# Optimization experiments

Measured on AMD Instinct MI355X. Metric: run time of the kernel, lower is better.

Reference implementation:

```python
import jax, jax.numpy as jnp
import numpy as np
from jax import lax

N, CIN, H, W = 4, 1024, 56, 56
CB = 256          # bottleneck channels
K = 9             # 3x3 kernel taps


def _conv(x, w, b, stride=1, padding='SAME'):
    y = lax.conv_general_dilated(x, w, (stride, stride), padding,
                                 dimension_numbers=('NCHW', 'OIHW', 'NCHW'))
    return y + b[None, :, None, None]


def _bilinear_gather(feat, ys, xs):
    # feat: [N,C,H,W]; ys, xs: [N,P] float sample coords. Zero padding outside.
    n, c, h, w = feat.shape
    y0 = jnp.floor(ys); x0 = jnp.floor(xs)
    wy1 = ys - y0; wy0 = 1.0 - wy1
    wx1 = xs - x0; wx0 = 1.0 - wx1
    flat = feat.reshape(n, c, h * w)

    def g(yi, xi):
        valid = (yi >= 0) & (yi <= h - 1) & (xi >= 0) & (xi <= w - 1)
        yc = jnp.clip(yi, 0, h - 1).astype(jnp.int32)
        xc = jnp.clip(xi, 0, w - 1).astype(jnp.int32)
        idx = (yc * w + xc)  # [N,P]
        vals = jnp.take_along_axis(flat, idx[:, None, :], axis=2)  # [N,C,P]
        return vals * valid[:, None, :].astype(feat.dtype)

    out = (g(y0, x0) * (wy0 * wx0)[:, None, :]
           + g(y0, x0 + 1) * (wy0 * wx1)[:, None, :]
           + g(y0 + 1, x0) * (wy1 * wx0)[:, None, :]
           + g(y0 + 1, x0 + 1) * (wy1 * wx1)[:, None, :])
    return out  # [N,C,P]


def _deform_conv3x3(feat, w, b, w_off, b_off):
    # DCNv1: offsets predicted by a standard 3x3 conv (18 = 2*K channels),
    # then bilinear-sample input at p + p_k + offset, accumulate with kernel w.
    n, c, h, ww = feat.shape
    off = _conv(feat, w_off, b_off)                 # [N, 2K, H, W]
    off = off.reshape(n, K, 2, h, ww)
    dy, dx = off[:, :, 0], off[:, :, 1]             # [N,K,H,W]
    ki, kj = jnp.meshgrid(jnp.arange(3), jnp.arange(3), indexing='ij')
    ky = (ki.reshape(-1) - 1).astype(feat.dtype)    # kernel dy offsets, rate=1
    kx = (kj.reshape(-1) - 1).astype(feat.dtype)
    hh = jnp.arange(h, dtype=feat.dtype)
    wc = jnp.arange(ww, dtype=feat.dtype)
    ys = hh[None, None, :, None] + ky[None, :, None, None] + dy   # [N,K,H,W]
    xs = wc[None, None, None, :] + kx[None, :, None, None] + dx
    sampled = _bilinear_gather(feat, ys.reshape(n, -1), xs.reshape(n, -1))
    sampled = sampled.reshape(n, c, K, h, ww)       # [N,C,K,H,W]
    out = jnp.einsum('nckhw,ock->nohw', sampled, w.reshape(w.shape[0], c, K))
    return out + b[None, :, None, None]


def setup_inputs() -> dict:
    key = jax.random.key(0)
    ks = jax.random.split(key, 6)
    x = jax.random.normal(ks[0], (N, CIN, H, W), dtype=jnp.float32)
    w1 = jax.random.normal(ks[1], (CB, CIN, 1, 1), dtype=jnp.float32) * 0.02
    b1 = jnp.zeros((CB,), jnp.float32)
    w_off = jax.random.normal(ks[2], (2 * K, CB, 3, 3), dtype=jnp.float32) * 0.01
    b_off = jnp.zeros((2 * K,), jnp.float32)
    w2 = jax.random.normal(ks[3], (CB, CB, 3, 3), dtype=jnp.float32) * 0.02
    b2 = jnp.zeros((CB,), jnp.float32)
    w3 = jax.random.normal(ks[4], (CIN, CB, 1, 1), dtype=jnp.float32) * 0.02
    b3 = jnp.zeros((CIN,), jnp.float32)
    return {"x": x, "w1": w1, "b1": b1, "w_off": w_off, "b_off": b_off,
            "w2": w2, "b2": b2, "w3": w3, "b3": b3}


def reference(x, w1, b1, w_off, b_off, w2, b2, w3, b3):
    # shortcut is identity (in_channels == out_channels, stride=1)
    r = jax.nn.relu(_conv(x, w1, b1))                      # conv1 1x1 + relu
    r = jax.nn.relu(_deform_conv3x3(r, w2, b2, w_off, b_off))  # deform 3x3 + relu
    r = _conv(r, w3, b3)                                   # conv3 1x1, no act
    return jax.nn.relu(x + r)
```

## Files before the change

kernel.cpp:

```cpp
#include <hip/hip_runtime.h>
#include <hip/hip_bf16.h>

#define N_   4
#define CIN  1024
#define H_   56
#define W_   56
#define HW   3136
#define CB   256
#define KK   9
#define OFFC 18

typedef __attribute__((ext_vector_type(8))) short short8;
typedef __attribute__((ext_vector_type(4))) short short4v;
typedef __attribute__((ext_vector_type(4))) float float4v;
typedef unsigned short ushort_t;

__device__ inline ushort_t bf16_rne(float f) {
    unsigned int u = __float_as_uint(f);
    unsigned int r = (u + 0x7FFFu + ((u >> 16) & 1u)) >> 16;
    return (ushort_t)r;
}
__device__ inline void split_bf16(float f, ushort_t& hi, ushort_t& lo) {
    ushort_t h = bf16_rne(f);
    float hf = __uint_as_float(((unsigned int)h) << 16);
    hi = h;
    lo = bf16_rne(f - hf);
}
__device__ inline short8 ld_frag_lds(const ushort_t* base) {
    short4v a = *(const short4v*)base;
    short4v b = *(const short4v*)(base + 4);
    return __builtin_shufflevector(a, b, 0, 1, 2, 3, 4, 5, 6, 7);
}
__device__ inline void lds_barrier() {
    asm volatile("s_waitcnt lgkmcnt(0)" ::: "memory");
    __builtin_amdgcn_s_barrier();
    __builtin_amdgcn_sched_barrier(0);
}

__global__ void __launch_bounds__(256) pack_weights_kernel(
    const float* __restrict__ w1, const float* __restrict__ w2,
    const float* __restrict__ w3, const float* __restrict__ w_off,
    ushort_t* __restrict__ w1p, ushort_t* __restrict__ w2p,
    ushort_t* __restrict__ w3p, ushort_t* __restrict__ wofp)
{
    int e = blockIdx.x * 256 + threadIdx.x;
    if (e < 256 * 1024) {
        int o = e >> 10, k = e & 1023;
        ushort_t hi, lo; split_bf16(w1[e], hi, lo);
        w1p[(size_t)(o * 2 + 0) * 1024 + k] = hi;
        w1p[(size_t)(o * 2 + 1) * 1024 + k] = lo;
        return;
    }
    e -= 256 * 1024;
    if (e < 256 * 256 * 9) {
        int o = e / 2304; int rem = e % 2304; int c = rem / 9; int k = rem % 9;
        w2p[(size_t)(k * 256 + o) * 256 + c] = bf16_rne(w2[e]);
        return;
    }
    e -= 256 * 256 * 9;
    if (e < 1024 * 256) {
        int o = e >> 8, k = e & 255;
        ushort_t hi, lo; split_bf16(w3[e], hi, lo);
        w3p[(size_t)(o * 2 + 0) * 256 + k] = hi;
        w3p[(size_t)(o * 2 + 1) * 256 + k] = lo;
        return;
    }
    e -= 1024 * 256;
    if (e < 9 * 32 * 256) {
        int k = e / (32 * 256);
        int rem = e % (32 * 256);
        int m = rem >> 8, c = rem & 255;
        float v = (m < OFFC) ? w_off[((size_t)m * 256 + c) * 9 + k] : 0.f;
        wofp[e] = bf16_rne(v);
    }
}

template <int MFRAG, bool RELU, bool RESID>
__global__ void __launch_bounds__(256, 4) conv1x1_mfma_kernel(
    const ushort_t* __restrict__ Wp,
    const float* __restrict__ Xin,
    const float* __restrict__ bias,
    const float* __restrict__ resid,
    float* __restrict__ Cout,
    int M, int Kdim)
{
    __shared__ ushort_t Bs[64][36];

    const int tid  = threadIdx.x;
    const int wave = tid >> 6;
    const int lane = tid & 63;
    const int l15  = lane & 15;
    const int quad = lane >> 4;
    const int pBase = blockIdx.x * 64;
    const int mBase = blockIdx.y * (MFRAG * 64) + wave * (MFRAG * 16);
    const int n     = blockIdx.z;
    const float* Xn = Xin + (size_t)n * Kdim * HW;

    float4v acc[MFRAG][4];
#pragma unroll
    for (int i = 0; i < MFRAG; ++i)
#pragma unroll
        for (int j = 0; j < 4; ++j) acc[i][j] = (float4v)(0.f);

    const int kk = tid >> 3;
    const int pq = (tid & 7) * 8;

    const float* src0 = &Xn[(size_t)kk * HW + pBase + pq];
    float4 c0 = *reinterpret_cast<const float4*>(src0);
    float4 c1 = *reinterpret_cast<const float4*>(src0 + 4);

    for (int k0 = 0; k0 < Kdim; k0 += 32) {
        lds_barrier();
        float vs[8] = {c0.x, c0.y, c0.z, c0.w, c1.x, c1.y, c1.z, c1.w};
#pragma unroll
        for (int j = 0; j < 8; ++j) Bs[pq + j][kk] = bf16_rne(vs[j]);

        short8 ah[MFRAG], al[MFRAG];
#pragma unroll
        for (int mt = 0; mt < MFRAG; ++mt) {
            const ushort_t* arow = Wp +
                ((size_t)(mBase + mt * 16 + l15) * 2) * Kdim + k0 + quad * 8;
            ah[mt] = *(const short8*)(arow);
            al[mt] = *(const short8*)(arow + Kdim);
        }
        if (k0 + 32 < Kdim) {
            const float* src = &Xn[(size_t)(k0 + 32 + kk) * HW + pBase + pq];
            c0 = *reinterpret_cast<const float4*>(src);
            c1 = *reinterpret_cast<const float4*>(src + 4);
        }
        lds_barrier();

        short8 bh[4];
#pragma unroll
        for (int nt = 0; nt < 4; ++nt)
            bh[nt] = ld_frag_lds(&Bs[nt * 16 + l15][quad * 8]);
        __builtin_amdgcn_s_setprio(1);
#pragma unroll
        for (int mt = 0; mt < MFRAG; ++mt)
#pragma unroll
            for (int nt = 0; nt < 4; ++nt) {
                acc[mt][nt] = __builtin_amdgcn_mfma_f32_16x16x32_bf16(
                    ah[mt], bh[nt], acc[mt][nt], 0, 0, 0);
                acc[mt][nt] = __builtin_amdgcn_mfma_f32_16x16x32_bf16(
                    al[mt], bh[nt], acc[mt][nt], 0, 0, 0);
            }
        __builtin_amdgcn_s_setprio(0);
    }

#pragma unroll
    for (int mt = 0; mt < MFRAG; ++mt)
#pragma unroll
        for (int rr = 0; rr < 4; ++rr) {
            int row = mBase + mt * 16 + quad * 4 + rr;
            float bv = bias[row];
#pragma unroll
            for (int nt = 0; nt < 4; ++nt) {
                int col = pBase + nt * 16 + l15;
                size_t idx = ((size_t)n * M + row) * HW + col;
                float v = acc[mt][nt][rr] + bv;
                if (RESID) v += resid[idx];
                if (RELU)  v = fmaxf(v, 0.f);
                Cout[idx] = v;
            }
        }
}

__global__ void __launch_bounds__(256, 2) offset_mfma_kernel(
    const float* __restrict__ r,
    const ushort_t* __restrict__ wofp,
    const float* __restrict__ b_off,
    float* __restrict__ off)
{
    __shared__ float win[32][174];

    const int tid  = threadIdx.x;
    const int h    = blockIdx.x;
    const int n    = blockIdx.y;
    const int wave = tid >> 6;
    const int lane = tid & 63;
    const int l15  = lane & 15;
    const int quad = lane >> 4;
    const float* rn = r + (size_t)n * CB * HW;

    const int p = wave * 16 + l15;

    float4v acc[2];
    acc[0] = (float4v)(0.f);
    acc[1] = (float4v)(0.f);

    for (int cb = 0; cb < CB; cb += 32) {
        __syncthreads();
        for (int f = tid; f < 32 * 3 * 14; f += 256) {
            int c = f / 42, remf = f % 42, row = remf / 14, x4 = (remf % 14) * 4;
            int yg = h - 1 + row;
            float4 v = {0.f, 0.f, 0.f, 0.f};
            if (yg >= 0 && yg < H_)
                v = *reinterpret_cast<const float4*>(
                    &rn[(size_t)(cb + c) * HW + yg * W_ + x4]);
            *reinterpret_cast<float4*>(&win[c][row * 56 + x4]) = v;
        }
        __syncthreads();

        short8 ahA0, ahA1, ahB0, ahB1;
        {
            const ushort_t* a0 = wofp + (size_t)(0 * 32 + l15) * 256 + cb + quad * 8;
            ahA0 = *(const short8*)a0;
            ahA1 = *(const short8*)(a0 + 16 * 256);
        }
#pragma unroll
        for (int k = 0; k < KK; ++k) {
            if (k + 1 < KK) {
                const ushort_t* a1 = wofp +
                    (size_t)((k + 1) * 32 + l15) * 256 + cb + quad * 8;
                ahB0 = *(const short8*)a1;
                ahB1 = *(const short8*)(a1 + 16 * 256);
            }
            const int ky = k / 3;
            const int dx = (k % 3) - 1;
            int x = p + dx;
            bool pvalid = (p < 56) && (x >= 0) && (x < 56);
            int xc = min(max(x, 0), 55);
            short8 bh;
#pragma unroll
            for (int j = 0; j < 8; ++j) {
                float v = win[quad * 8 + j][ky * 56 + xc];
                bh[j] = (short)bf16_rne(pvalid ? v : 0.f);
            }
            acc[0] = __builtin_amdgcn_mfma_f32_16x16x32_bf16(
                ahA0, bh, acc[0], 0, 0, 0);
            acc[1] = __builtin_amdgcn_mfma_f32_16x16x32_bf16(
                ahA1, bh, acc[1], 0, 0, 0);
            ahA0 = ahB0; ahA1 = ahB1;
        }
    }

    if (p < 56) {
#pragma unroll
        for (int mt = 0; mt < 2; ++mt)
#pragma unroll
            for (int rr = 0; rr < 4; ++rr) {
                int m = mt * 16 + quad * 4 + rr;
                if (m < OFFC)
                    off[((size_t)n * OFFC + m) * HW + h * W_ + p] =
                        acc[mt][rr] + b_off[m];
            }
    }
}

#define TPX   28
#define WROWS 5
#define WCOLS 36
#define WPOS  (WROWS * WCOLS)
#define CSTR  33
#define WITEMS (32 * WROWS * 9)
#define DBLK  (H_ * 2 * N_)
#define NCHUNK 8

__global__ void __launch_bounds__(512, 2) deform_mfma_kernel(
    const float* __restrict__ r,
    const float* __restrict__ off,
    const ushort_t* __restrict__ w2p,
    const float* __restrict__ b2,
    float* __restrict__ r2)
{
    __shared__ float    win[WPOS][CSTR];
    __shared__ ushort_t Bs[2][KK][32][36];

    const int tid = threadIdx.x;
    const int bid = blockIdx.x;
    const int swz = (bid & 7) * (DBLK >> 3) + (bid >> 3);
    const int xh  = swz & 1;
    const int h   = (swz >> 1) % H_;
    const int n   = swz / (H_ * 2);
    const int xb  = xh * TPX;
    const float* rn   = r + (size_t)n * CB * HW;
    const float* offn = off + (size_t)n * OFFC * HW;

    int   bi0 = 0, bi1 = 0, bi2 = 0, bi3 = 0;
    float bw0 = 0.f, bw1 = 0.f, bw2 = 0.f, bw3 = 0.f;
    int   go0 = 0, go1 = 0, go2 = 0, go3 = 0;
    bool  bfast = true;
    const bool bactive = (tid < 288);
    const int  bk = bactive ? (tid / 32) : 0;
    const int  bp = bactive ? (tid % 32) : 0;
    if (bactive && bp < TPX) {
        int pg = xb + bp;
        float dy = offn[(size_t)(2 * bk) * HW + h * W_ + pg];
        float dx = offn[(size_t)(2 * bk + 1) * HW + h * W_ + pg];
        float ys = (float)(h + (bk / 3) - 1) + dy;
        float xs = (float)(pg + (bk % 3) - 1) + dx;
        float y0f = floorf(ys), x0f = floorf(xs);
        int y0 = (int)y0f, x0 = (int)x0f;
        float wy1 = ys - y0f, wy0 = 1.f - wy1;
        float wx1 = xs - x0f, wx0 = 1.f - wx1;
        int   wid[4]; float wg[4]; int gof[4]; bool fast = true;
#pragma unroll
        for (int u = 0; u < 2; ++u)
#pragma unroll
            for (int vv = 0; vv < 2; ++vv) {
                int yy = y0 + u, xx = x0 + vv;
                bool valid = (yy >= 0) && (yy <= 55) && (xx >= 0) && (xx <= 55);
                float wgt = valid ? (u ? wy1 : wy0) * (vv ? wx1 : wx0) : 0.f;
                int ry = yy - (h - 2);
                int rx = xx - (xb - 4);
                if (wgt != 0.f &&
                    (ry < 0 || ry >= WROWS || rx < 0 || rx >= WCOLS))
                    fast = false;
                int idx = min(max(ry, 0), WROWS - 1) * WCOLS +
                          min(max(rx, 0), WCOLS - 1);
                wid[u * 2 + vv] = idx;
                wg[u * 2 + vv]  = wgt;
                gof[u * 2 + vv] = valid ? (yy * W_ + xx) : 0;
            }
        bfast = fast;
        bi0 = wid[0]; bi1 = wid[1]; bi2 = wid[2]; bi3 = wid[3];
        bw0 = wg[0];  bw1 = wg[1];  bw2 = wg[2];  bw3 = wg[3];
        go0 = gof[0]; go1 = gof[1]; go2 = gof[2]; go3 = gof[3];
    }

    const int wave = tid >> 6;
    const int lane = tid & 63;
    const int l15  = lane & 15;
    const int quad = lane >> 4;
    const int mW   = wave * 32;

    float4v acc[2][2];
#pragma unroll
    for (int i = 0; i < 2; ++i)
#pragma unroll
        for (int j = 0; j < 2; ++j) acc[i][j] = (float4v)(0.f);

    auto wload = [&](int f, int cbg) -> float4 {
        int c = f / 45, remf = f % 45, row = remf / 9, q = remf % 9;
        int yg = min(max(h - 2 + row, 0), H_ - 1);
        int xg = xb - 4 + q * 4;
        const float* src = &rn[(size_t)(cbg + c) * HW + yg * W_];
        float4 v;
        if (xg >= 0 && xg <= W_ - 4) {
            v = *reinterpret_cast<const float4*>(src + xg);
        } else {
            v.x = src[min(max(xg + 0, 0), W_ - 1)];
            v.y = src[min(max(xg + 1, 0), W_ - 1)];
            v.z = src[min(max(xg + 2, 0), W_ - 1)];
            v.w = src[min(max(xg + 3, 0), W_ - 1)];
        }
        return v;
    };
    auto wwrite = [&](float4* pre) {
#pragma unroll
        for (int i = 0; i < 3; ++i) {
            int f = tid + 512 * i;
            if (f < WITEMS) {
                int c = f / 45, remf = f % 45, row = remf / 9, q = remf % 9;
                int pos = row * WCOLS + q * 4;
                float4 v = pre[i];
                win[pos + 0][c] = v.x;
                win[pos + 1][c] = v.y;
                win[pos + 2][c] = v.z;
                win[pos + 3][c] = v.w;
            }
        }
    };
    auto build = [&](int cbg, int pb) {
#pragma unroll
        for (int c4 = 0; c4 < 32; c4 += 4) {
            float s[4];
            if (bfast) {
#pragma unroll
                for (int j = 0; j < 4; ++j) {
                    int c = c4 + j;
                    s[j] = bw0 * win[bi0][c] + bw1 * win[bi1][c] +
                           bw2 * win[bi2][c] + bw3 * win[bi3][c];
                }
            } else {
#pragma unroll
                for (int j = 0; j < 4; ++j) {
                    const float* rc = rn + (size_t)(cbg + c4 + j) * HW;
                    s[j] = bw0 * rc[go0] + bw1 * rc[go1] +
                           bw2 * rc[go2] + bw3 * rc[go3];
                }
            }
            short4v pk;
#pragma unroll
            for (int j = 0; j < 4; ++j) pk[j] = (short)bf16_rne(s[j]);
            *(short4v*)&Bs[pb][bk][bp][c4] = pk;
        }
    };

    float4 pre[3];
#pragma unroll
    for (int i = 0; i < 3; ++i) {
        int f = tid + 512 * i;
        if (f < WITEMS) pre[i] = wload(f, 0);
    }
    wwrite(pre);
#pragma unroll
    for (int i = 0; i < 3; ++i) {
        int f = tid + 512 * i;
        if (f < WITEMS) pre[i] = wload(f, 32);
    }
    lds_barrier();
    if (bactive) build(0, 0);
    lds_barrier();

    for (int ci = 0; ci < NCHUNK; ++ci) {
        const int cb = ci * 32;
        const bool hasNext = (ci + 1 < NCHUNK);
        if (hasNext) {
            wwrite(pre);
            if (ci + 2 < NCHUNK) {
#pragma unroll
                for (int i = 0; i < 3; ++i) {
                    int f = tid + 512 * i;
                    if (f < WITEMS) pre[i] = wload(f, cb + 64);
                }
            }
            lds_barrier();
            if (bactive) build(cb + 32, (ci + 1) & 1);
        }

        const ushort_t* bsb = &Bs[ci & 1][0][0][0];
        __builtin_amdgcn_s_setprio(1);
#pragma unroll
        for (int k = 0; k < KK; ++k) {
            short8 ah[2];
#pragma unroll
            for (int mt = 0; mt < 2; ++mt) {
                const ushort_t* arow = w2p +
                    (size_t)(k * 256 + (mW + mt * 16 + l15)) * 256 +
                    cb + quad * 8;
                ah[mt] = *(const short8*)(arow);
            }
            short8 bh[2];
#pragma unroll
            for (int nt = 0; nt < 2; ++nt)
                bh[nt] = ld_frag_lds(bsb + ((size_t)k * 32 +
                         nt * 16 + l15) * 36 + quad * 8);
#pragma unroll
            for (int mt = 0; mt < 2; ++mt)
#pragma unroll
                for (int nt = 0; nt < 2; ++nt)
                    acc[mt][nt] = __builtin_amdgcn_mfma_f32_16x16x32_bf16(
                        ah[mt], bh[nt], acc[mt][nt], 0, 0, 0);
        }
        __builtin_amdgcn_s_setprio(0);
        if (hasNext) lds_barrier();
    }

#pragma unroll
    for (int mt = 0; mt < 2; ++mt)
#pragma unroll
        for (int rr = 0; rr < 4; ++rr) {
            int o = mW + mt * 16 + quad * 4 + rr;
            float bv = b2[o];
#pragma unroll
            for (int nt = 0; nt < 2; ++nt) {
                int p = nt * 16 + l15;
                if (p < TPX) {
                    float v = fmaxf(acc[mt][nt][rr] + bv, 0.f);
                    r2[((size_t)n * CB + o) * HW + h * W_ + xb + p] = v;
                }
            }
        }
}

extern "C" void kernel_launch(void* const* d_in, const int* in_sizes, int n_in,
                              void* d_out, int out_size, void* d_ws, size_t ws_size,
                              hipStream_t stream)
{
    const float* x     = (const float*)d_in[0];
    const float* w1    = (const float*)d_in[1];
    const float* b1    = (const float*)d_in[2];
    const float* w_off = (const float*)d_in[3];
    const float* b_off = (const float*)d_in[4];
    const float* w2    = (const float*)d_in[5];
    const float* b2    = (const float*)d_in[6];
    const float* w3    = (const float*)d_in[7];
    const float* b3    = (const float*)d_in[8];
    float* out = (float*)d_out;

    float* ws  = (float*)d_ws;
    float* r    = ws;
    float* r2   = r  + (size_t)N_ * CB * HW;
    float* offb = r2 + (size_t)N_ * CB * HW;
    ushort_t* w1p  = (ushort_t*)(offb + (size_t)N_ * OFFC * HW);
    ushort_t* w2p  = w1p + (size_t)256 * 2 * 1024;
    ushort_t* w3p  = w2p + (size_t)9 * 256 * 256;
    ushort_t* wofp = w3p + (size_t)1024 * 2 * 256;

    {
        int total = 256 * 1024 + 256 * 256 * 9 + 1024 * 256 + 9 * 32 * 256;
        pack_weights_kernel<<<(total + 255) / 256, 256, 0, stream>>>(
            w1, w2, w3, w_off, w1p, w2p, w3p, wofp);
    }
    {
        dim3 grid(HW / 64, CB / 128, N_);
        conv1x1_mfma_kernel<2, true, false><<<grid, 256, 0, stream>>>(
            w1p, x, b1, nullptr, r, CB, CIN);
    }
    {
        dim3 grid(H_, N_);
        offset_mfma_kernel<<<grid, 256, 0, stream>>>(r, wofp, b_off, offb);
    }
    {
        deform_mfma_kernel<<<DBLK, 512, 0, stream>>>(r, offb, w2p, b2, r2);
    }
    {
        dim3 grid(HW / 64, CIN / 128, N_);
        conv1x1_mfma_kernel<2, true, true><<<grid, 256, 0, stream>>>(
            w3p, r2, b3, x, out, CIN, CB);
    }
}
```

Before: 341.6 us.

## Split offset conv over input-channel halves and shrink conv1 M tile

The offset conv grid is split along input channels into two halves, doubling its block count from 224 to 448. Each half writes its own partial sum buffer, and the deform kernel adds the two partials plus the bias when it reads the offsets. Separately, conv1 now uses a 64-row M tile instead of 128, which also doubles its block count and should fill the GPU better. The cost is an extra partial-offset buffer with the extra reads that come with it, and more redundant loading of B tiles in conv1.

```diff
diff --git a/kernel.cpp b/kernel.cpp
--- a/kernel.cpp
+++ b/kernel.cpp
@@ -168,19 +168,20 @@
 __global__ void __launch_bounds__(256, 2) offset_mfma_kernel(
     const float* __restrict__ r,
     const ushort_t* __restrict__ wofp,
-    const float* __restrict__ b_off,
-    float* __restrict__ off)
+    float* __restrict__ offp)
 {
     __shared__ float win[32][174];
 
     const int tid  = threadIdx.x;
     const int h    = blockIdx.x;
-    const int n    = blockIdx.y;
+    const int kh   = blockIdx.y;
+    const int n    = blockIdx.z;
     const int wave = tid >> 6;
     const int lane = tid & 63;
     const int l15  = lane & 15;
     const int quad = lane >> 4;
     const float* rn = r + (size_t)n * CB * HW;
+    const int cb0 = kh * 128;
 
     const int p = wave * 16 + l15;
 
@@ -188,7 +189,7 @@
     acc[0] = (float4v)(0.f);
     acc[1] = (float4v)(0.f);
 
-    for (int cb = 0; cb < CB; cb += 32) {
+    for (int cb = cb0; cb < cb0 + 128; cb += 32) {
         __syncthreads();
         for (int f = tid; f < 32 * 3 * 14; f += 256) {
             int c = f / 42, remf = f % 42, row = remf / 14, x4 = (remf % 14) * 4;
@@ -235,14 +236,14 @@
     }
 
     if (p < 56) {
+        float* base = offp + (size_t)(kh * N_ + n) * OFFC * HW;
 #pragma unroll
         for (int mt = 0; mt < 2; ++mt)
 #pragma unroll
             for (int rr = 0; rr < 4; ++rr) {
                 int m = mt * 16 + quad * 4 + rr;
                 if (m < OFFC)
-                    off[((size_t)n * OFFC + m) * HW + h * W_ + p] =
-                        acc[mt][rr] + b_off[m];
+                    base[(size_t)m * HW + h * W_ + p] = acc[mt][rr];
             }
     }
 }
@@ -259,6 +260,7 @@
 __global__ void __launch_bounds__(512, 2) deform_mfma_kernel(
     const float* __restrict__ r,
     const float* __restrict__ off,
+    const float* __restrict__ b_off,
     const ushort_t* __restrict__ w2p,
     const float* __restrict__ b2,
     float* __restrict__ r2)
@@ -273,8 +275,9 @@
     const int h   = (swz >> 1) % H_;
     const int n   = swz / (H_ * 2);
     const int xb  = xh * TPX;
-    const float* rn   = r + (size_t)n * CB * HW;
-    const float* offn = off + (size_t)n * OFFC * HW;
+    const float* rn    = r + (size_t)n * CB * HW;
+    const float* offn0 = off + (size_t)n * OFFC * HW;
+    const float* offn1 = off + (size_t)(N_ + n) * OFFC * HW;
 
     int   bi0 = 0, bi1 = 0, bi2 = 0, bi3 = 0;
     float bw0 = 0.f, bw1 = 0.f, bw2 = 0.f, bw3 = 0.f;
@@ -285,8 +288,10 @@
     const int  bp = bactive ? (tid % 32) : 0;
     if (bactive && bp < TPX) {
         int pg = xb + bp;
-        float dy = offn[(size_t)(2 * bk) * HW + h * W_ + pg];
-        float dx = offn[(size_t)(2 * bk + 1) * HW + h * W_ + pg];
+        size_t iy = (size_t)(2 * bk) * HW + h * W_ + pg;
+        size_t ix = (size_t)(2 * bk + 1) * HW + h * W_ + pg;
+        float dy = offn0[iy] + offn1[iy] + b_off[2 * bk];
+        float dx = offn0[ix] + offn1[ix] + b_off[2 * bk + 1];
         float ys = (float)(h + (bk / 3) - 1) + dy;
         float xs = (float)(pg + (bk % 3) - 1) + dx;
         float y0f = floorf(ys), x0f = floorf(xs);
@@ -483,7 +488,7 @@
     float* r    = ws;
     float* r2   = r  + (size_t)N_ * CB * HW;
     float* offb = r2 + (size_t)N_ * CB * HW;
-    ushort_t* w1p  = (ushort_t*)(offb + (size_t)N_ * OFFC * HW);
+    ushort_t* w1p  = (ushort_t*)(offb + (size_t)2 * N_ * OFFC * HW);
     ushort_t* w2p  = w1p + (size_t)256 * 2 * 1024;
     ushort_t* w3p  = w2p + (size_t)9 * 256 * 256;
     ushort_t* wofp = w3p + (size_t)1024 * 2 * 256;
@@ -494,16 +499,17 @@
             w1, w2, w3, w_off, w1p, w2p, w3p, wofp);
     }
     {
-        dim3 grid(HW / 64, CB / 128, N_);
-        conv1x1_mfma_kernel<2, true, false><<<grid, 256, 0, stream>>>(
+        dim3 grid(HW / 64, CB / 64, N_);
+        conv1x1_mfma_kernel<1, true, false><<<grid, 256, 0, stream>>>(
             w1p, x, b1, nullptr, r, CB, CIN);
     }
     {
-        dim3 grid(H_, N_);
-        offset_mfma_kernel<<<grid, 256, 0, stream>>>(r, wofp, b_off, offb);
+        dim3 grid(H_, 2, N_);
+        offset_mfma_kernel<<<grid, 256, 0, stream>>>(r, wofp, offb);
     }
     {
-        deform_mfma_kernel<<<DBLK, 512, 0, stream>>>(r, offb, w2p, b2, r2);
+        deform_mfma_kernel<<<DBLK, 512, 0, stream>>>(
+            r, offb, b_off, w2p, b2, r2);
     }
     {
         dim3 grid(HW / 64, CIN / 128, N_);
```

After: 333.8 us. 2.3% less time.
